# Optimization experiments

Hardware: AMD Instinct MI355X
Metric: run time of the kernel (lower is better)

The kernel has to match this reference:

```python
import jax, jax.numpy as jnp
import numpy as np

B, L, S, H, E, D = 4, 2048, 2048, 8, 64, 64

def setup_inputs() -> dict:
    key = jax.random.key(0)
    kq, kk, kv = jax.random.split(key, 3)
    queries = jax.random.normal(kq, (B, L, H, E), dtype=jnp.float32)
    keys = jax.random.normal(kk, (B, S, H, E), dtype=jnp.float32)
    values = jax.random.normal(kv, (B, S, H, D), dtype=jnp.float32)
    return {"queries": queries, "keys": keys, "values": values}

def reference(queries, keys, values):
    # scale = self.scale or 1/sqrt(E)
    scale = 1.0 / jnp.sqrt(jnp.float32(queries.shape[-1]))
    # scores: [B, H, L, S]
    scores = jnp.einsum('blhe,bshe->bhls', queries, keys)
    # dropout is identity at inference (Keras Dropout only active in training)
    A = jax.nn.softmax(scale * scores, axis=-1)
    # output: [B, L, H, D]
    return jnp.einsum('bhls,bshd->blhd', A, values)
```

## Files before the change

kernel.cpp:

```cpp
#include <hip/hip_runtime.h>


#define B_ 4
#define L_ 2048
#define S_ 2048
#define H_ 8

#define NUMSZ (B_ * L_ * H_ * 64)
#define LSZ (B_ * L_ * H_)
#define KVELEM (B_ * H_ * S_ * 64)
#define TILE_ELEMS 2048

typedef __attribute__((ext_vector_type(8))) __bf16 bf16x8;
typedef __attribute__((ext_vector_type(4))) __bf16 bf16x4;
typedef __attribute__((ext_vector_type(16))) float floatx16;

union BF4U { bf16x4 v; uint2 u; };
union BF8U { bf16x8 v; uint4 u; };

__device__ __forceinline__ void async_load16(const void* g, void* l) {
  __builtin_amdgcn_global_load_lds(
      (const __attribute__((address_space(1))) unsigned int*)g,
      (__attribute__((address_space(3))) unsigned int*)l, 16, 0, 0);
}

__device__ __forceinline__ bf16x8 cvt8(float4 a, float4 b) {
  bf16x8 r;
  r[0] = (__bf16)a.x; r[1] = (__bf16)a.y; r[2] = (__bf16)a.z; r[3] = (__bf16)a.w;
  r[4] = (__bf16)b.x; r[5] = (__bf16)b.y; r[6] = (__bf16)b.z; r[7] = (__bf16)b.w;
  return r;
}

__device__ __forceinline__ void softmax_pb(const floatx16& sc, int h32, float& l,
                                           bf16x8& pB0v, bf16x8& pB1v) {
  BF4U pg[4];
#pragma unroll
  for (int g = 0; g < 4; ++g) {
    float p0 = __builtin_amdgcn_exp2f(sc[4 * g + 0]);
    float p1 = __builtin_amdgcn_exp2f(sc[4 * g + 1]);
    float p2 = __builtin_amdgcn_exp2f(sc[4 * g + 2]);
    float p3 = __builtin_amdgcn_exp2f(sc[4 * g + 3]);
    l += (p0 + p1) + (p2 + p3);
    pg[g].v = (bf16x4){(__bf16)p0, (__bf16)p1, (__bf16)p2, (__bf16)p3};
  }
  uint2 sendA = h32 ? pg[0].u : pg[1].u;
  uint2 sendB = h32 ? pg[2].u : pg[3].u;
  uint2 recvA, recvB;
  recvA.x = __shfl_xor((int)sendA.x, 32);
  recvA.y = __shfl_xor((int)sendA.y, 32);
  recvB.x = __shfl_xor((int)sendB.x, 32);
  recvB.y = __shfl_xor((int)sendB.y, 32);
  BF8U pB0, pB1;
  if (h32 == 0) {
    pB0.u = (uint4){pg[0].u.x, pg[0].u.y, recvA.x, recvA.y};
    pB1.u = (uint4){pg[2].u.x, pg[2].u.y, recvB.x, recvB.y};
  } else {
    pB0.u = (uint4){recvA.x, recvA.y, pg[1].u.x, pg[1].u.y};
    pB1.u = (uint4){recvB.x, recvB.y, pg[3].u.x, pg[3].u.y};
  }
  pB0v = pB0.v;
  pB1v = pB1.v;
}

__global__ __launch_bounds__(256) void prep_kernel(const float* __restrict__ K,
                                                   const float* __restrict__ V,
                                                   __bf16* __restrict__ Kb,
                                                   __bf16* __restrict__ Vb) {
  __shared__ float Vs[32 * 64];
  const int bid = blockIdx.x;
  const int xcd = bid & 7;
  const int idx = bid >> 3;
  const int pair = xcd * 4 + (idx >> 6);
  const int tile = idx & 63;
  const int h = pair & 7;
  const int b = pair >> 3;
  const int obid = pair * 64 + tile;
  const int s0 = tile * 32;
  const int i = threadIdx.x;

  {
    const int s = i >> 3, cp = i & 7;
    const int e0 = 8 * (cp ^ (s & 7));
    const float* src = K + (((size_t)(b * S_ + s0 + s) * H_ + h) * 64 + e0);
    float4 a = *(const float4*)src;
    float4 bb = *(const float4*)(src + 4);
    *(bf16x8*)(Kb + (size_t)obid * TILE_ELEMS + i * 8) = cvt8(a, bb);
  }
  {
    const int s = i >> 3, d0 = (i & 7) * 8;
    const float* src = V + (((size_t)(b * S_ + s0 + s) * H_ + h) * 64 + d0);
    float4 a = *(const float4*)src;
    float4 bb = *(const float4*)(src + 4);
    *(float4*)&Vs[s * 64 + d0] = a;
    *(float4*)&Vs[s * 64 + d0 + 4] = bb;
  }
  __syncthreads();
  {
    const int Ll = i >> 3, cp = i & 7;
    const int ci = cp ^ (Ll & 7);
    const int d = 2 * Ll + (ci >> 2);
    const int ch = ci & 3;
    BF8U o;
#pragma unroll
    for (int j = 0; j < 8; ++j) o.v[j] = (__bf16)Vs[(8 * ch + j) * 64 + d];
    *(bf16x8*)(Vb + (size_t)obid * TILE_ELEMS + i * 8) = o.v;
  }
}

__global__ __launch_bounds__(256, 2) void attn_kernel(const float* __restrict__ Q,
                                                      const __bf16* __restrict__ Kb,
                                                      const __bf16* __restrict__ Vb,
                                                      float* __restrict__ O,
                                                      float* __restrict__ num_ws,
                                                      float* __restrict__ l_ws,
                                                      int splits) {
  __shared__ __align__(16) __bf16 Kt[2][2 * TILE_ELEMS];
  __shared__ __align__(16) __bf16 Vt[2][2 * TILE_ELEMS];

  const int tid = threadIdx.x;
  const int lane = tid & 63;
  const int wave = tid >> 6;
  const int q32 = lane & 31;
  const int h32 = lane >> 5;

  const int bid = blockIdx.x;
  const int xcd = bid & 7;
  const int idx = bid >> 3;
  const int bs = 8 * splits;
  const int pairl = idx / bs;
  const int sub = idx - pairl * bs;
  const int pair = xcd * 4 + pairl;
  const int qb = sub & 7;
  const int split = sub >> 3;
  const int h = pair & 7;
  const int b = pair >> 3;

  const int NT2 = (S_ / 32) / splits / 2;
  const int tile0 = split * NT2 * 2;

  const float qscale = 0.125f * 1.44269504088896340736f;
  const int qrow0 = qb * 256 + wave * 64 + q32;
  bf16x8 qf[2][4];
#pragma unroll
  for (int g = 0; g < 2; ++g) {
    const float* qp = Q + ((size_t)(b * L_ + qrow0 + g * 32) * H_ + h) * 64;
#pragma unroll
    for (int c = 0; c < 4; ++c) {
      const float* p = qp + c * 16 + h32 * 8;
      float4 a = *(const float4*)p;
      float4 bb = *(const float4*)(p + 4);
      float t[8] = {a.x, a.y, a.z, a.w, bb.x, bb.y, bb.z, bb.w};
#pragma unroll
      for (int j = 0; j < 8; ++j) qf[g][c][j] = (__bf16)(t[j] * qscale);
    }
  }

  int koff[4];
#pragma unroll
  for (int c = 0; c < 4; ++c) koff[c] = (q32 * 8 + (((2 * c + h32) ^ (q32 & 7)))) * 8;
  int voff[2][2];
#pragma unroll
  for (int s2 = 0; s2 < 2; ++s2)
#pragma unroll
    for (int dt = 0; dt < 2; ++dt) {
      int dp = dt * 32 + q32;
      int Ll = dp >> 1;
      int ci = (dp & 1) * 4 + 2 * s2 + h32;
      voff[s2][dt] = (Ll * 8 + (ci ^ (Ll & 7))) * 8;
    }

  float l[2] = {0.f, 0.f};
  floatx16 ot[2][2];
#pragma unroll
  for (int g = 0; g < 2; ++g)
#pragma unroll
    for (int r = 0; r < 16; ++r) { ot[g][0][r] = 0.f; ot[g][1][r] = 0.f; }

  const __bf16* KbBH = Kb + (size_t)(pair * 64) * TILE_ELEMS;
  const __bf16* VbBH = Vb + (size_t)(pair * 64) * TILE_ELEMS;
  const int lin8 = (wave * 64 + lane) * 8;

#pragma unroll
  for (int st = 0; st < 2; ++st) {
    async_load16(KbBH + (size_t)(tile0 + st) * TILE_ELEMS + lin8,
                 &Kt[0][st * TILE_ELEMS + wave * 512]);
    async_load16(VbBH + (size_t)(tile0 + st) * TILE_ELEMS + lin8,
                 &Vt[0][st * TILE_ELEMS + wave * 512]);
  }

  for (int t = 0; t < NT2; ++t) {
    const int buf = t & 1;
    __syncthreads();

    if (t + 1 < NT2) {
#pragma unroll
      for (int st = 0; st < 2; ++st) {
        async_load16(KbBH + (size_t)(tile0 + 2 * (t + 1) + st) * TILE_ELEMS + lin8,
                     &Kt[buf ^ 1][st * TILE_ELEMS + wave * 512]);
        async_load16(VbBH + (size_t)(tile0 + 2 * (t + 1) + st) * TILE_ELEMS + lin8,
                     &Vt[buf ^ 1][st * TILE_ELEMS + wave * 512]);
      }
    }

#pragma unroll
    for (int sb = 0; sb < 2; ++sb) {
      const __bf16* Kbuf = &Kt[buf][sb * TILE_ELEMS];
      const __bf16* Vbuf = &Vt[buf][sb * TILE_ELEMS];

      bf16x8 kA[4];
#pragma unroll
      for (int c = 0; c < 4; ++c) kA[c] = *(const bf16x8*)&Kbuf[koff[c]];

      floatx16 sc0, sc1;
#pragma unroll
      for (int r = 0; r < 16; ++r) { sc0[r] = 0.f; sc1[r] = 0.f; }
#pragma unroll
      for (int c = 0; c < 4; ++c)
        sc0 = __builtin_amdgcn_mfma_f32_32x32x16_bf16(kA[c], qf[0][c], sc0, 0, 0, 0);
#pragma unroll
      for (int c = 0; c < 4; ++c)
        sc1 = __builtin_amdgcn_mfma_f32_32x32x16_bf16(kA[c], qf[1][c], sc1, 0, 0, 0);

      bf16x8 p00, p01, p10, p11;
      softmax_pb(sc0, h32, l[0], p00, p01);
      softmax_pb(sc1, h32, l[1], p10, p11);

      bf16x8 vA[4];
      vA[0] = *(const bf16x8*)&Vbuf[voff[0][0]];
      vA[1] = *(const bf16x8*)&Vbuf[voff[0][1]];
      vA[2] = *(const bf16x8*)&Vbuf[voff[1][0]];
      vA[3] = *(const bf16x8*)&Vbuf[voff[1][1]];
      ot[0][0] = __builtin_amdgcn_mfma_f32_32x32x16_bf16(vA[0], p00, ot[0][0], 0, 0, 0);
      ot[0][1] = __builtin_amdgcn_mfma_f32_32x32x16_bf16(vA[1], p00, ot[0][1], 0, 0, 0);
      ot[1][0] = __builtin_amdgcn_mfma_f32_32x32x16_bf16(vA[0], p10, ot[1][0], 0, 0, 0);
      ot[1][1] = __builtin_amdgcn_mfma_f32_32x32x16_bf16(vA[1], p10, ot[1][1], 0, 0, 0);
      ot[0][0] = __builtin_amdgcn_mfma_f32_32x32x16_bf16(vA[2], p01, ot[0][0], 0, 0, 0);
      ot[0][1] = __builtin_amdgcn_mfma_f32_32x32x16_bf16(vA[3], p01, ot[0][1], 0, 0, 0);
      ot[1][0] = __builtin_amdgcn_mfma_f32_32x32x16_bf16(vA[2], p11, ot[1][0], 0, 0, 0);
      ot[1][1] = __builtin_amdgcn_mfma_f32_32x32x16_bf16(vA[3], p11, ot[1][1], 0, 0, 0);
    }
  }

#pragma unroll
  for (int g = 0; g < 2; ++g) {
    float lg = l[g] + __shfl_xor(l[g], 32);
    const int qrow = qrow0 + g * 32;
    if (splits == 1) {
      const float inv = 1.0f / lg;
      float* orow = O + ((size_t)(b * L_ + qrow) * H_ + h) * 64;
#pragma unroll
      for (int dt = 0; dt < 2; ++dt)
#pragma unroll
        for (int gg = 0; gg < 4; ++gg) {
          float4 v = {ot[g][dt][4 * gg + 0] * inv, ot[g][dt][4 * gg + 1] * inv,
                      ot[g][dt][4 * gg + 2] * inv, ot[g][dt][4 * gg + 3] * inv};
          *(float4*)(orow + dt * 32 + gg * 8 + h32 * 4) = v;
        }
    } else {
      float* nrow =
          num_ws + (size_t)split * NUMSZ + ((size_t)(b * L_ + qrow) * H_ + h) * 64;
#pragma unroll
      for (int dt = 0; dt < 2; ++dt)
#pragma unroll
        for (int gg = 0; gg < 4; ++gg) {
          float4 v = {ot[g][dt][4 * gg + 0], ot[g][dt][4 * gg + 1],
                      ot[g][dt][4 * gg + 2], ot[g][dt][4 * gg + 3]};
          *(float4*)(nrow + dt * 32 + gg * 8 + h32 * 4) = v;
        }
      if (h32 == 0)
        l_ws[(size_t)split * LSZ + (size_t)(b * L_ + qrow) * H_ + h] = lg;
    }
  }
}

__global__ __launch_bounds__(256) void combine_kernel(const float* __restrict__ num_ws,
                                                      const float* __restrict__ l_ws,
                                                      float* __restrict__ O, int splits) {
  const size_t i4 = ((size_t)blockIdx.x * 256 + threadIdx.x) * 4;
  float4 acc = {0.f, 0.f, 0.f, 0.f};
  float lt = 0.f;
  for (int s = 0; s < splits; ++s) {
    float4 v = *(const float4*)(num_ws + (size_t)s * NUMSZ + i4);
    acc.x += v.x; acc.y += v.y; acc.z += v.z; acc.w += v.w;
    lt += l_ws[(size_t)s * LSZ + (i4 >> 6)];
  }
  const float inv = 1.0f / lt;
  float4 o = {acc.x * inv, acc.y * inv, acc.z * inv, acc.w * inv};
  *(float4*)(O + i4) = o;
}

extern "C" void kernel_launch(void* const* d_in, const int* in_sizes, int n_in,
                              void* d_out, int out_size, void* d_ws, size_t ws_size,
                              hipStream_t stream) {
  const float* Q = (const float*)d_in[0];
  const float* K = (const float*)d_in[1];
  const float* V = (const float*)d_in[2];
  float* O = (float*)d_out;

  __bf16* Kb = (__bf16*)d_ws;
  __bf16* Vb = Kb + KVELEM;
  float* num_ws = (float*)(Vb + KVELEM);
  const size_t base = (size_t)2 * KVELEM * sizeof(__bf16);
  const size_t per_split = ((size_t)NUMSZ + (size_t)LSZ) * sizeof(float);
  int splits = 1;
  if (ws_size >= base + 4 * per_split) splits = 4;
  else if (ws_size >= base + 2 * per_split) splits = 2;
  float* l_ws = num_ws + (size_t)splits * NUMSZ;

  prep_kernel<<<B_ * H_ * 64, 256, 0, stream>>>(K, V, Kb, Vb);
  dim3 grid(B_ * H_ * (L_ / 256) * splits);
  attn_kernel<<<grid, 256, 0, stream>>>(Q, Kb, Vb, O, num_ws, l_ws, splits);
  if (splits > 1) {
    combine_kernel<<<NUMSZ / 4 / 256, 256, 0, stream>>>(num_ws, l_ws, O, splits);
  }
}
```

Baseline: 150.8 us.

## Halve per-block query rows, raise occupancy, and prioritize MFMA issue

Each wave now handles 32 query rows instead of 64, so a block covers 128 rows. The grid doubles and the launch bound goes from 2 to 3 blocks per CU, which cuts register pressure and should allow more concurrent waves to hide latency. s_setprio is wrapped around the MFMA sequences so waves issuing matrix ops get scheduling priority. The trade-off is that each K/V tile loaded into LDS is reused across half as many query rows, so global and LDS traffic per unit of compute roughly doubles.

```diff
diff --git a/kernel.cpp b/kernel.cpp
--- a/kernel.cpp
+++ b/kernel.cpp
@@ -107,7 +107,7 @@
   }
 }
 
-__global__ __launch_bounds__(256, 2) void attn_kernel(const float* __restrict__ Q,
+__global__ __launch_bounds__(256, 3) void attn_kernel(const float* __restrict__ Q,
                                                       const __bf16* __restrict__ Kb,
                                                       const __bf16* __restrict__ Vb,
                                                       float* __restrict__ O,
@@ -126,12 +126,12 @@
   const int bid = blockIdx.x;
   const int xcd = bid & 7;
   const int idx = bid >> 3;
-  const int bs = 8 * splits;
+  const int bs = 16 * splits;
   const int pairl = idx / bs;
   const int sub = idx - pairl * bs;
   const int pair = xcd * 4 + pairl;
-  const int qb = sub & 7;
-  const int split = sub >> 3;
+  const int qb = sub & 15;
+  const int split = sub >> 4;
   const int h = pair & 7;
   const int b = pair >> 3;
 
@@ -139,11 +139,10 @@
   const int tile0 = split * NT2 * 2;
 
   const float qscale = 0.125f * 1.44269504088896340736f;
-  const int qrow0 = qb * 256 + wave * 64 + q32;
-  bf16x8 qf[2][4];
-#pragma unroll
-  for (int g = 0; g < 2; ++g) {
-    const float* qp = Q + ((size_t)(b * L_ + qrow0 + g * 32) * H_ + h) * 64;
+  const int qrow = qb * 128 + wave * 32 + q32;
+  bf16x8 qf[4];
+  {
+    const float* qp = Q + ((size_t)(b * L_ + qrow) * H_ + h) * 64;
 #pragma unroll
     for (int c = 0; c < 4; ++c) {
       const float* p = qp + c * 16 + h32 * 8;
@@ -151,7 +150,7 @@
       float4 bb = *(const float4*)(p + 4);
       float t[8] = {a.x, a.y, a.z, a.w, bb.x, bb.y, bb.z, bb.w};
 #pragma unroll
-      for (int j = 0; j < 8; ++j) qf[g][c][j] = (__bf16)(t[j] * qscale);
+      for (int j = 0; j < 8; ++j) qf[c][j] = (__bf16)(t[j] * qscale);
     }
   }
 
@@ -169,12 +168,10 @@
       voff[s2][dt] = (Ll * 8 + (ci ^ (Ll & 7))) * 8;
     }
 
-  float l[2] = {0.f, 0.f};
-  floatx16 ot[2][2];
-#pragma unroll
-  for (int g = 0; g < 2; ++g)
-#pragma unroll
-    for (int r = 0; r < 16; ++r) { ot[g][0][r] = 0.f; ot[g][1][r] = 0.f; }
+  float l = 0.f;
+  floatx16 ot[2];
+#pragma unroll
+  for (int r = 0; r < 16; ++r) { ot[0][r] = 0.f; ot[1][r] = 0.f; }
 
   const __bf16* KbBH = Kb + (size_t)(pair * 64) * TILE_ELEMS;
   const __bf16* VbBH = Vb + (size_t)(pair * 64) * TILE_ELEMS;
@@ -211,40 +208,34 @@
 #pragma unroll
       for (int c = 0; c < 4; ++c) kA[c] = *(const bf16x8*)&Kbuf[koff[c]];
 
-      floatx16 sc0, sc1;
-#pragma unroll
-      for (int r = 0; r < 16; ++r) { sc0[r] = 0.f; sc1[r] = 0.f; }
+      floatx16 sc;
+#pragma unroll
+      for (int r = 0; r < 16; ++r) sc[r] = 0.f;
+      __builtin_amdgcn_s_setprio(1);
 #pragma unroll
       for (int c = 0; c < 4; ++c)
-        sc0 = __builtin_amdgcn_mfma_f32_32x32x16_bf16(kA[c], qf[0][c], sc0, 0, 0, 0);
-#pragma unroll
-      for (int c = 0; c < 4; ++c)
-        sc1 = __builtin_amdgcn_mfma_f32_32x32x16_bf16(kA[c], qf[1][c], sc1, 0, 0, 0);
-
-      bf16x8 p00, p01, p10, p11;
-      softmax_pb(sc0, h32, l[0], p00, p01);
-      softmax_pb(sc1, h32, l[1], p10, p11);
+        sc = __builtin_amdgcn_mfma_f32_32x32x16_bf16(kA[c], qf[c], sc, 0, 0, 0);
+      __builtin_amdgcn_s_setprio(0);
+
+      bf16x8 p0, p1;
+      softmax_pb(sc, h32, l, p0, p1);
 
       bf16x8 vA[4];
       vA[0] = *(const bf16x8*)&Vbuf[voff[0][0]];
       vA[1] = *(const bf16x8*)&Vbuf[voff[0][1]];
       vA[2] = *(const bf16x8*)&Vbuf[voff[1][0]];
       vA[3] = *(const bf16x8*)&Vbuf[voff[1][1]];
-      ot[0][0] = __builtin_amdgcn_mfma_f32_32x32x16_bf16(vA[0], p00, ot[0][0], 0, 0, 0);
-      ot[0][1] = __builtin_amdgcn_mfma_f32_32x32x16_bf16(vA[1], p00, ot[0][1], 0, 0, 0);
-      ot[1][0] = __builtin_amdgcn_mfma_f32_32x32x16_bf16(vA[0], p10, ot[1][0], 0, 0, 0);
-      ot[1][1] = __builtin_amdgcn_mfma_f32_32x32x16_bf16(vA[1], p10, ot[1][1], 0, 0, 0);
-      ot[0][0] = __builtin_amdgcn_mfma_f32_32x32x16_bf16(vA[2], p01, ot[0][0], 0, 0, 0);
-      ot[0][1] = __builtin_amdgcn_mfma_f32_32x32x16_bf16(vA[3], p01, ot[0][1], 0, 0, 0);
-      ot[1][0] = __builtin_amdgcn_mfma_f32_32x32x16_bf16(vA[2], p11, ot[1][0], 0, 0, 0);
-      ot[1][1] = __builtin_amdgcn_mfma_f32_32x32x16_bf16(vA[3], p11, ot[1][1], 0, 0, 0);
-    }
-  }
-
-#pragma unroll
-  for (int g = 0; g < 2; ++g) {
-    float lg = l[g] + __shfl_xor(l[g], 32);
-    const int qrow = qrow0 + g * 32;
+      __builtin_amdgcn_s_setprio(1);
+      ot[0] = __builtin_amdgcn_mfma_f32_32x32x16_bf16(vA[0], p0, ot[0], 0, 0, 0);
+      ot[1] = __builtin_amdgcn_mfma_f32_32x32x16_bf16(vA[1], p0, ot[1], 0, 0, 0);
+      ot[0] = __builtin_amdgcn_mfma_f32_32x32x16_bf16(vA[2], p1, ot[0], 0, 0, 0);
+      ot[1] = __builtin_amdgcn_mfma_f32_32x32x16_bf16(vA[3], p1, ot[1], 0, 0, 0);
+      __builtin_amdgcn_s_setprio(0);
+    }
+  }
+
+  {
+    float lg = l + __shfl_xor(l, 32);
     if (splits == 1) {
       const float inv = 1.0f / lg;
       float* orow = O + ((size_t)(b * L_ + qrow) * H_ + h) * 64;
@@ -252,8 +243,8 @@
       for (int dt = 0; dt < 2; ++dt)
 #pragma unroll
         for (int gg = 0; gg < 4; ++gg) {
-          float4 v = {ot[g][dt][4 * gg + 0] * inv, ot[g][dt][4 * gg + 1] * inv,
-                      ot[g][dt][4 * gg + 2] * inv, ot[g][dt][4 * gg + 3] * inv};
+          float4 v = {ot[dt][4 * gg + 0] * inv, ot[dt][4 * gg + 1] * inv,
+                      ot[dt][4 * gg + 2] * inv, ot[dt][4 * gg + 3] * inv};
           *(float4*)(orow + dt * 32 + gg * 8 + h32 * 4) = v;
         }
     } else {
@@ -263,8 +254,8 @@
       for (int dt = 0; dt < 2; ++dt)
 #pragma unroll
         for (int gg = 0; gg < 4; ++gg) {
-          float4 v = {ot[g][dt][4 * gg + 0], ot[g][dt][4 * gg + 1],
-                      ot[g][dt][4 * gg + 2], ot[g][dt][4 * gg + 3]};
+          float4 v = {ot[dt][4 * gg + 0], ot[dt][4 * gg + 1],
+                      ot[dt][4 * gg + 2], ot[dt][4 * gg + 3]};
           *(float4*)(nrow + dt * 32 + gg * 8 + h32 * 4) = v;
         }
       if (h32 == 0)
@@ -308,7 +299,7 @@
   float* l_ws = num_ws + (size_t)splits * NUMSZ;
 
   prep_kernel<<<B_ * H_ * 64, 256, 0, stream>>>(K, V, Kb, Vb);
-  dim3 grid(B_ * H_ * (L_ / 256) * splits);
+  dim3 grid(B_ * H_ * (L_ / 128) * splits);
   attn_kernel<<<grid, 256, 0, stream>>>(Q, Kb, Vb, O, num_ws, l_ws, splits);
   if (splits > 1) {
     combine_kernel<<<NUMSZ / 4 / 256, 256, 0, stream>>>(num_ws, l_ws, O, splits);
```

Measured after the change: 152.3 us. Within noise of the previous version (+1.0%).
